# Performance work log

Measured on AMD Instinct MI355X. Metric: run time of the kernel, lower is better.

The kernel has to match this reference:

```python
import jax, jax.numpy as jnp
import numpy as np

D_MODEL = 512
N_HEADS = 8
HEAD_DIM = D_MODEL // N_HEADS
KV_RANK = 128
B, T = 8, 4096


def _rope(x):
    # x: (B, H, T, D); non-interleaved half rotation as in the source
    d = x.shape[-1]
    half = d // 2
    freq = 1.0 / (10000.0 ** (jnp.arange(half, dtype=jnp.float32) / half))
    t = jnp.arange(x.shape[2], dtype=jnp.float32)
    freqs = jnp.einsum('i,j->ij', t, freq)          # (T, half)
    cos_f = jnp.cos(freqs)[None, None, :, :]
    sin_f = jnp.sin(freqs)[None, None, :, :]
    x1, x2 = jnp.split(x, 2, axis=-1)
    return jnp.concatenate([x1 * cos_f - x2 * sin_f, x1 * sin_f + x2 * cos_f], axis=-1)


def setup_inputs() -> dict:
    key = jax.random.key(0)
    ks = jax.random.split(key, 9)
    s = lambda fan_in: 1.0 / np.sqrt(fan_in)
    return {
        'x':  jax.random.normal(ks[0], (B, T, D_MODEL), dtype=jnp.float32),
        'Wq': jax.random.normal(ks[1], (D_MODEL, D_MODEL), dtype=jnp.float32) * s(D_MODEL),
        'bq': jnp.zeros((D_MODEL,), dtype=jnp.float32),
        'Wd': jax.random.normal(ks[2], (D_MODEL, KV_RANK), dtype=jnp.float32) * s(D_MODEL),
        'bd': jnp.zeros((KV_RANK,), dtype=jnp.float32),
        'Wu': jax.random.normal(ks[3], (KV_RANK, D_MODEL * 2), dtype=jnp.float32) * s(KV_RANK),
        'bu': jnp.zeros((D_MODEL * 2,), dtype=jnp.float32),
        'Wo': jax.random.normal(ks[4], (D_MODEL, D_MODEL), dtype=jnp.float32) * s(D_MODEL),
        'bo': jnp.zeros((D_MODEL,), dtype=jnp.float32),
    }


def reference(x, Wq, bq, Wd, bd, Wu, bu, Wo, bo):
    b, t, _ = x.shape
    q = (x @ Wq + bq).reshape(b, t, N_HEADS, HEAD_DIM).transpose(0, 2, 1, 3)   # (B,H,T,D)
    kv = ((x @ Wd + bd) @ Wu + bu).reshape(b, t, N_HEADS, 2 * HEAD_DIM)
    k, v = jnp.split(kv, 2, axis=-1)
    k = k.transpose(0, 2, 1, 3)                                                # (B,H,T,D)
    v = v.transpose(0, 2, 1, 3)
    q = jax.nn.elu(_rope(q)) + 1.0
    k = jax.nn.elu(_rope(k)) + 1.0
    context = jnp.einsum('bhtd,bhte->bhde', k, v)      # (B,H,D,D)
    out = jnp.einsum('bhtd,bhde->bhte', q, context)    # (B,H,T,D)
    k_sum = k.sum(axis=2)                              # (B,H,D)
    z = 1.0 / (jnp.einsum('bhtd,bhd->bht', q, k_sum) + 1e-6)
    out = out * z[..., None]
    out = out.transpose(0, 2, 1, 3).reshape(b, t, D_MODEL)
    return out @ Wo + bo
```

## Files before the change

kernel.cpp:

```cpp
#include <hip/hip_runtime.h>
#include <math.h>

#define T_SEQ 4096
#define BATCH 8
#define DM    512
#define NH    8
#define HD    64
#define RANK  128
#define NCHUNK 8
#define MTOT  (BATCH * T_SEQ)
#define BK 64

typedef unsigned int u32;
typedef unsigned short u16;
using bf16x8  = __attribute__((ext_vector_type(8))) __bf16;
using floatx4 = __attribute__((ext_vector_type(4))) float;

__device__ __forceinline__ u16 f2bf(float f) {
  u32 u = __float_as_uint(f);
  u32 r = (u + 0x7FFFu + ((u >> 16) & 1u)) >> 16;
  return (u16)r;
}
__device__ __forceinline__ void hilo(float f, u16& h, u16& l) {
  h = f2bf(f);
  float hf = __uint_as_float(((u32)h) << 16);
  l = f2bf(f - hf);
}
__device__ __forceinline__ float elu1(float x) {
  return (x > 0.f) ? x + 1.f : expf(x);
}
__device__ __forceinline__ void async16(void* lds, const void* g) {
  __builtin_amdgcn_global_load_lds(
      (const __attribute__((address_space(1))) u32*)g,
      (__attribute__((address_space(3))) u32*)lds, 16, 0, 0);
}
__device__ __forceinline__ bf16x8 fragld(const u16* base, int row, int kk, int quad) {
  int ch = (kk * 4 + quad) ^ (row & 7);
  return *(const bf16x8*)((const char*)base + row * 128 + ch * 16);
}

__global__ void cs_kernel(float2* __restrict__ cs) {
  int i = blockIdx.x * 256 + threadIdx.x;
  if (i >= T_SEQ * 32) return;
  int t = i >> 5, d = i & 31;
  double freq = pow(10000.0, -(double)d / 32.0);
  double a = (double)t * freq;
  cs[i] = make_float2((float)cos(a), (float)sin(a));
}

__global__ __launch_bounds__(256) void pack_bf16(const float* __restrict__ x,
                                                 u16* __restrict__ y) {
  int i = blockIdx.x * 256 + threadIdx.x;
  const float4 v = ((const float4*)x)[i];
  ushort4 o;
  o.x = f2bf(v.x); o.y = f2bf(v.y); o.z = f2bf(v.z); o.w = f2bf(v.w);
  ((ushort4*)y)[i] = o;
}

__global__ __launch_bounds__(256) void transpose_cast(const float* __restrict__ W,
                                                      u16* __restrict__ WT,
                                                      int K, int N) {
  __shared__ float t[32][33];
  int kb = blockIdx.x * 32, nb = blockIdx.y * 32;
  int tx = threadIdx.x & 31, tg = threadIdx.x >> 5;
#pragma unroll
  for (int i = 0; i < 4; i++)
    t[tg * 4 + i][tx] = W[(size_t)(kb + tg * 4 + i) * N + nb + tx];
  __syncthreads();
#pragma unroll
  for (int i = 0; i < 4; i++)
    WT[(size_t)(nb + tg * 4 + i) * K + kb + tx] = f2bf(t[tx][tg * 4 + i]);
}

__global__ __launch_bounds__(256) void transpose_cast_hilo(
    const float* __restrict__ W, u16* __restrict__ WTh, u16* __restrict__ WTl,
    int K, int N) {
  __shared__ float t[32][33];
  int kb = blockIdx.x * 32, nb = blockIdx.y * 32;
  int tx = threadIdx.x & 31, tg = threadIdx.x >> 5;
#pragma unroll
  for (int i = 0; i < 4; i++)
    t[tg * 4 + i][tx] = W[(size_t)(kb + tg * 4 + i) * N + nb + tx];
  __syncthreads();
#pragma unroll
  for (int i = 0; i < 4; i++) {
    u16 h, l;
    hilo(t[tx][tg * 4 + i], h, l);
    WTh[(size_t)(nb + tg * 4 + i) * K + kb + tx] = h;
    WTl[(size_t)(nb + tg * 4 + i) * K + kb + tx] = l;
  }
}

template <bool BF16OUT>
__global__ __launch_bounds__(256) void gemm_bf16_bt(
    const u16* __restrict__ A, const u16* __restrict__ BT,
    const float* __restrict__ bias, void* __restrict__ Cv,
    int M, int N, int K) {
  __shared__ u16 As[128 * BK];
  __shared__ u16 Bs[128 * BK];
  const int tid = threadIdx.x;
  const int lane = tid & 63, w = tid >> 6;
  const int m0 = blockIdx.y * 128, n0 = blockIdx.x * 128;
  const int wm = (w & 1) * 64, wn = (w >> 1) * 64;
  const int srow = lane >> 3, schunk = lane & 7;
  const int lane15 = lane & 15, quad = lane >> 4;
  floatx4 acc[4][4] = {};
  for (int kt = 0; kt < K; kt += BK) {
    __syncthreads();
#pragma unroll
    for (int i = 0; i < 4; i++) {
      int R = (w * 4 + i) * 8 + srow;
      int cg = schunk ^ (R & 7);
      async16((char*)As + (w * 4 + i) * 1024,
              (const char*)A + ((size_t)(m0 + R) * K + kt) * 2 + cg * 16);
      async16((char*)Bs + (w * 4 + i) * 1024,
              (const char*)BT + ((size_t)(n0 + R) * K + kt) * 2 + cg * 16);
    }
    __syncthreads();
#pragma unroll
    for (int kk = 0; kk < 2; kk++) {
      bf16x8 af[4], bfr[4];
#pragma unroll
      for (int mi = 0; mi < 4; mi++) af[mi] = fragld(As, wm + mi * 16 + lane15, kk, quad);
#pragma unroll
      for (int ni = 0; ni < 4; ni++) bfr[ni] = fragld(Bs, wn + ni * 16 + lane15, kk, quad);
#pragma unroll
      for (int mi = 0; mi < 4; mi++)
#pragma unroll
        for (int ni = 0; ni < 4; ni++)
          acc[mi][ni] = __builtin_amdgcn_mfma_f32_16x16x32_bf16(
              af[mi], bfr[ni], acc[mi][ni], 0, 0, 0);
    }
  }
#pragma unroll
  for (int mi = 0; mi < 4; mi++) {
    int row = m0 + wm + mi * 16 + (quad << 2);
#pragma unroll
    for (int ni = 0; ni < 4; ni++) {
      int col = n0 + wn + ni * 16 + lane15;
      float bb = bias[col];
#pragma unroll
      for (int r = 0; r < 4; r++) {
        float v = acc[mi][ni][r] + bb;
        if (BF16OUT) ((u16*)Cv)[(size_t)(row + r) * N + col] = f2bf(v);
        else         ((float*)Cv)[(size_t)(row + r) * N + col] = v;
      }
    }
  }
}

__global__ __launch_bounds__(256) void gemm_wd_hilo(
    const u16* __restrict__ A, const u16* __restrict__ BT,
    const float* __restrict__ bias, u16* __restrict__ Ch, u16* __restrict__ Cl,
    int M, int N, int K) {
  __shared__ u16 As[128 * BK];
  __shared__ u16 Bs[128 * BK];
  const int tid = threadIdx.x;
  const int lane = tid & 63, w = tid >> 6;
  const int m0 = blockIdx.y * 128, n0 = blockIdx.x * 128;
  const int wm = (w & 1) * 64, wn = (w >> 1) * 64;
  const int srow = lane >> 3, schunk = lane & 7;
  const int lane15 = lane & 15, quad = lane >> 4;
  floatx4 acc[4][4] = {};
  for (int kt = 0; kt < K; kt += BK) {
    __syncthreads();
#pragma unroll
    for (int i = 0; i < 4; i++) {
      int R = (w * 4 + i) * 8 + srow;
      int cg = schunk ^ (R & 7);
      async16((char*)As + (w * 4 + i) * 1024,
              (const char*)A + ((size_t)(m0 + R) * K + kt) * 2 + cg * 16);
      async16((char*)Bs + (w * 4 + i) * 1024,
              (const char*)BT + ((size_t)(n0 + R) * K + kt) * 2 + cg * 16);
    }
    __syncthreads();
#pragma unroll
    for (int kk = 0; kk < 2; kk++) {
      bf16x8 af[4], bfr[4];
#pragma unroll
      for (int mi = 0; mi < 4; mi++) af[mi] = fragld(As, wm + mi * 16 + lane15, kk, quad);
#pragma unroll
      for (int ni = 0; ni < 4; ni++) bfr[ni] = fragld(Bs, wn + ni * 16 + lane15, kk, quad);
#pragma unroll
      for (int mi = 0; mi < 4; mi++)
#pragma unroll
        for (int ni = 0; ni < 4; ni++)
          acc[mi][ni] = __builtin_amdgcn_mfma_f32_16x16x32_bf16(
              af[mi], bfr[ni], acc[mi][ni], 0, 0, 0);
    }
  }
#pragma unroll
  for (int mi = 0; mi < 4; mi++) {
    int row = m0 + wm + mi * 16 + (quad << 2);
#pragma unroll
    for (int ni = 0; ni < 4; ni++) {
      int col = n0 + wn + ni * 16 + lane15;
      float bb = bias[col];
#pragma unroll
      for (int r = 0; r < 4; r++) {
        float v = acc[mi][ni][r] + bb;
        u16 hh, ll;
        hilo(v, hh, ll);
        size_t idx = (size_t)(row + r) * N + col;
        Ch[idx] = hh;
        Cl[idx] = ll;
      }
    }
  }
}

__global__ __launch_bounds__(256) void ctx_fused(
    const u16* __restrict__ Chi, const u16* __restrict__ Clo,
    const u16* __restrict__ Wuh, const u16* __restrict__ Wul,
    const float* __restrict__ bu, const float2* __restrict__ cs,
    float* __restrict__ ctxp, float* __restrict__ ksump) {
  __shared__ __align__(16) u16 uni[16384];
  __shared__ __align__(16) u16 Bh[128 * 64], Bl[128 * 64];
  __shared__ float bus[128];
  __shared__ float ksl[256];
  const int tid = threadIdx.x;
  const int lane = tid & 63, w = tid >> 6;
  const int lane15 = lane & 15, quad = lane >> 4;
  const int chunk = blockIdx.x, bh = blockIdx.y;
  const int b = bh >> 3, h = bh & 7;
  u16* Ah = uni;
  u16* Al = uni + 4096;
  u16* Kh = uni;
  u16* Kl = uni + 4096;
  u16* Vh = uni + 8192;
  u16* Vl = uni + 12288;
  if (tid < 128) bus[tid] = bu[h * RANK + tid];
  floatx4 acc2[4] = {};
  float ksacc[4] = {0.f, 0.f, 0.f, 0.f};
  for (int tile = 0; tile < 8; tile++) {
    const int t0 = chunk * 512 + tile * 64;
    floatx4 acc[8] = {};
#pragma unroll
    for (int rp = 0; rp < 2; rp++) {
      __syncthreads();
#pragma unroll
      for (int i = 0; i < 2; i++) {
        int R = (w * 2 + i) * 8 + (lane >> 3);
        int cg = (lane & 7) ^ (R & 7);
        size_t aoff = ((size_t)(b * T_SEQ + t0 + R) * RANK + rp * 64) * 2 + cg * 16;
        async16((char*)Ah + (w * 2 + i) * 1024, (const char*)Chi + aoff);
        async16((char*)Al + (w * 2 + i) * 1024, (const char*)Clo + aoff);
      }
#pragma unroll
      for (int i = 0; i < 4; i++) {
        int R = (w * 4 + i) * 8 + (lane >> 3);
        int cg = (lane & 7) ^ (R & 7);
        size_t boff = ((size_t)(h * 128 + R) * RANK + rp * 64) * 2 + cg * 16;
        async16((char*)Bh + (w * 4 + i) * 1024, (const char*)Wuh + boff);
        async16((char*)Bl + (w * 4 + i) * 1024, (const char*)Wul + boff);
      }
      __syncthreads();
#pragma unroll
      for (int kk = 0; kk < 2; kk++) {
        bf16x8 ah  = fragld(Ah, w * 16 + lane15, kk, quad);
        bf16x8 al8 = fragld(Al, w * 16 + lane15, kk, quad);
#pragma unroll
        for (int ni = 0; ni < 8; ni++) {
          bf16x8 bh8 = fragld(Bh, ni * 16 + lane15, kk, quad);
          bf16x8 bl8 = fragld(Bl, ni * 16 + lane15, kk, quad);
          acc[ni] = __builtin_amdgcn_mfma_f32_16x16x32_bf16(ah,  bh8, acc[ni], 0, 0, 0);
          acc[ni] = __builtin_amdgcn_mfma_f32_16x16x32_bf16(ah,  bl8, acc[ni], 0, 0, 0);
          acc[ni] = __builtin_amdgcn_mfma_f32_16x16x32_bf16(al8, bh8, acc[ni], 0, 0, 0);
          acc[ni] = __builtin_amdgcn_mfma_f32_16x16x32_bf16(al8, bl8, acc[ni], 0, 0, 0);
        }
      }
    }
    __syncthreads();
    {
      const int tloc = w * 16 + (quad << 2);
      const int tg = t0 + tloc;
      const int chq = w * 2 + (quad >> 1);
      const int half8 = (quad & 1) * 8;
#pragma unroll
      for (int ni = 0; ni < 2; ni++) {
        int d = ni * 16 + lane15;
        float b1 = bus[d], b2 = bus[d + 32];
        ushort4 khl, kll, khh, klh;
        float s0 = 0.f, s1 = 0.f;
#pragma unroll
        for (int r = 0; r < 4; r++) {
          float2 sc = cs[(size_t)(tg + r) * 32 + d];
          float x1 = acc[ni][r] + b1;
          float x2 = acc[ni + 2][r] + b2;
          float k1 = elu1(x1 * sc.x - x2 * sc.y);
          float k2 = elu1(x1 * sc.y + x2 * sc.x);
          s0 += k1; s1 += k2;
          u16 hh, ll;
          hilo(k1, hh, ll); ((u16*)&khl)[r] = hh; ((u16*)&kll)[r] = ll;
          hilo(k2, hh, ll); ((u16*)&khh)[r] = hh; ((u16*)&klh)[r] = ll;
        }
        ksacc[ni] += s0; ksacc[ni + 2] += s1;
        int offd = d * 128 + ((chq ^ (d & 7)) << 4) + half8;
        *(ushort4*)((char*)Kh + offd)              = khl;
        *(ushort4*)((char*)Kl + offd)              = kll;
        *(ushort4*)((char*)Kh + offd + 32 * 128)   = khh;
        *(ushort4*)((char*)Kl + offd + 32 * 128)   = klh;
      }
#pragma unroll
      for (int ni = 4; ni < 8; ni++) {
        int e = (ni - 4) * 16 + lane15;
        float be = bus[64 + e];
        ushort4 vh4, vl4;
#pragma unroll
        for (int r = 0; r < 4; r++) {
          u16 hh, ll;
          hilo(acc[ni][r] + be, hh, ll);
          ((u16*)&vh4)[r] = hh; ((u16*)&vl4)[r] = ll;
        }
        int off = e * 128 + ((chq ^ (e & 7)) << 4) + half8;
        *(ushort4*)((char*)Vh + off) = vh4;
        *(ushort4*)((char*)Vl + off) = vl4;
      }
    }
    __syncthreads();
#pragma unroll
    for (int kk = 0; kk < 2; kk++) {
      bf16x8 kh8 = fragld(Kh, w * 16 + lane15, kk, quad);
      bf16x8 kl8 = fragld(Kl, w * 16 + lane15, kk, quad);
#pragma unroll
      for (int ni = 0; ni < 4; ni++) {
        bf16x8 vh8 = fragld(Vh, ni * 16 + lane15, kk, quad);
        bf16x8 vl8 = fragld(Vl, ni * 16 + lane15, kk, quad);
        acc2[ni] = __builtin_amdgcn_mfma_f32_16x16x32_bf16(kh8, vh8, acc2[ni], 0, 0, 0);
        acc2[ni] = __builtin_amdgcn_mfma_f32_16x16x32_bf16(kh8, vl8, acc2[ni], 0, 0, 0);
        acc2[ni] = __builtin_amdgcn_mfma_f32_16x16x32_bf16(kl8, vh8, acc2[ni], 0, 0, 0);
        acc2[ni] = __builtin_amdgcn_mfma_f32_16x16x32_bf16(kl8, vl8, acc2[ni], 0, 0, 0);
      }
    }
  }
  const size_t obase = ((size_t)bh * NCHUNK + chunk) * 4096;
#pragma unroll
  for (int ni = 0; ni < 4; ni++)
#pragma unroll
    for (int r = 0; r < 4; r++)
      ctxp[obase + (size_t)(w * 16 + (quad << 2) + r) * 64 + ni * 16 + lane15] = acc2[ni][r];
  for (int g = 0; g < 4; g++) {
    __syncthreads();
    ksl[tid] = ksacc[g];
    __syncthreads();
    if (tid < 16) {
      float s = 0.f;
#pragma unroll
      for (int j = 0; j < 16; j++) s += ksl[(j >> 2) * 64 + (j & 3) * 16 + tid];
      ksump[(bh * NCHUNK + chunk) * 64 + g * 16 + tid] = s;
    }
  }
}

__global__ __launch_bounds__(256) void reduce_kernel(
    const float* __restrict__ ctxp, const float* __restrict__ ksump,
    float* __restrict__ ctx, float* __restrict__ ksum) {
  int bh = blockIdx.x, tid = threadIdx.x;
  for (int i = tid; i < 4096; i += 256) {
    float s = 0.f;
    for (int c = 0; c < NCHUNK; c++) s += ctxp[(size_t)(bh * NCHUNK + c) * 4096 + i];
    ctx[(size_t)bh * 4096 + i] = s;
  }
  if (tid < 64) {
    float s = 0.f;
    for (int c = 0; c < NCHUNK; c++) s += ksump[(bh * NCHUNK + c) * 64 + tid];
    ksum[bh * 64 + tid] = s;
  }
}

__global__ __launch_bounds__(256) void out_kernel(
    const float* __restrict__ Q, const float* __restrict__ ctx,
    const float* __restrict__ ksum, const float2* __restrict__ cs,
    u16* __restrict__ attn) {
  __shared__ __align__(16) float Qs[128 * 68];
  __shared__ __align__(16) float Cts[64 * 68];
  __shared__ float ks[64];
  __shared__ float zs[128];
  const int tid = threadIdx.x;
  const int tt0 = blockIdx.x * 128;
  const int bh = blockIdx.y;
  const int b = bh >> 3, h = bh & 7;
  for (int i = tid; i < 4096; i += 256)
    Cts[(i >> 6) * 68 + (i & 63)] = ctx[(size_t)bh * 4096 + i];
  if (tid < 64) ks[tid] = ksum[bh * 64 + tid];
  for (int i = tid; i < 8192; i += 256) {
    int t = i >> 6, d = i & 63;
    Qs[t * 68 + d] = Q[(size_t)(b * T_SEQ + tt0 + t) * DM + h * HD + d];
  }
  __syncthreads();
  for (int i = tid; i < 128 * 32; i += 256) {
    int t = i >> 5, d = i & 31;
    float x1 = Qs[t * 68 + d], x2 = Qs[t * 68 + d + 32];
    float2 sc = cs[(size_t)(tt0 + t) * 32 + d];
    float r1 = x1 * sc.x - x2 * sc.y;
    float r2 = x1 * sc.y + x2 * sc.x;
    Qs[t * 68 + d]      = (r1 > 0.f) ? r1 + 1.f : expf(r1);
    Qs[t * 68 + d + 32] = (r2 > 0.f) ? r2 + 1.f : expf(r2);
  }
  __syncthreads();
  if (tid < 128) {
    float z = 0.f;
#pragma unroll 8
    for (int d = 0; d < 64; d++) z += Qs[tid * 68 + d] * ks[d];
    zs[tid] = 1.f / (z + 1e-6f);
  }
  __syncthreads();
  const int tx = tid & 15, ty = tid >> 4;
  float acc[8][4] = {};
  for (int d = 0; d < 64; d++) {
    const float4 c4 = *(const float4*)&Cts[d * 68 + tx * 4];
#pragma unroll
    for (int i = 0; i < 8; i++) {
      float q = Qs[(ty * 8 + i) * 68 + d];
      acc[i][0] += q * c4.x; acc[i][1] += q * c4.y;
      acc[i][2] += q * c4.z; acc[i][3] += q * c4.w;
    }
  }
#pragma unroll
  for (int i = 0; i < 8; i++) {
    int t = ty * 8 + i;
    float zz = zs[t];
    ushort4 o;
    o.x = f2bf(acc[i][0] * zz); o.y = f2bf(acc[i][1] * zz);
    o.z = f2bf(acc[i][2] * zz); o.w = f2bf(acc[i][3] * zz);
    *(ushort4*)&attn[(size_t)(b * T_SEQ + tt0 + t) * DM + h * HD + tx * 4] = o;
  }
}

extern "C" void kernel_launch(void* const* d_in, const int* in_sizes, int n_in,
                              void* d_out, int out_size, void* d_ws, size_t ws_size,
                              hipStream_t stream) {
  const float* x  = (const float*)d_in[0];
  const float* Wq = (const float*)d_in[1];
  const float* bq = (const float*)d_in[2];
  const float* Wd = (const float*)d_in[3];
  const float* bd = (const float*)d_in[4];
  const float* Wu = (const float*)d_in[5];
  const float* bu = (const float*)d_in[6];
  const float* Wo = (const float*)d_in[7];
  const float* bo = (const float*)d_in[8];
  float* out = (float*)d_out;

  float* ws = (float*)d_ws;
  size_t o_cs   = 0;
  size_t o_Q    = o_cs + (size_t)T_SEQ * 32 * 2;
  size_t o_Chi  = o_Q + (size_t)MTOT * DM;
  size_t o_Clo  = o_Chi + (size_t)MTOT * RANK / 2;
  size_t o_ctxp = o_Clo + (size_t)MTOT * RANK / 2;
  size_t o_ksp  = o_ctxp + (size_t)64 * NCHUNK * 4096;
  size_t o_ctx  = o_ksp + (size_t)64 * NCHUNK * 64;
  size_t o_ks   = o_ctx + (size_t)64 * 4096;
  size_t o_xbf  = o_ks + 64 * 64;
  size_t o_wqT  = o_xbf + (size_t)MTOT * DM / 2;
  size_t o_wdT  = o_wqT + (size_t)DM * DM / 2;
  size_t o_woT  = o_wdT + (size_t)DM * RANK / 2;
  size_t o_wuTh = o_woT + (size_t)DM * DM / 2;
  size_t o_wuTl = o_wuTh + (size_t)(2 * DM) * RANK / 2;
  size_t total  = o_wuTl + (size_t)(2 * DM) * RANK / 2;
  if (ws_size < total * sizeof(float)) return;

  float2* cs  = (float2*)(ws + o_cs);
  float* Qb   = ws + o_Q;
  u16* Chi    = (u16*)(ws + o_Chi);
  u16* Clo    = (u16*)(ws + o_Clo);
  float* ctxp = ws + o_ctxp;
  float* ksp  = ws + o_ksp;
  float* ctxf = ws + o_ctx;
  float* ksf  = ws + o_ks;
  u16* x_bf   = (u16*)(ws + o_xbf);
  u16* attn_bf= x_bf;
  u16* WqT    = (u16*)(ws + o_wqT);
  u16* WdT    = (u16*)(ws + o_wdT);
  u16* WoT    = (u16*)(ws + o_woT);
  u16* WuTh   = (u16*)(ws + o_wuTh);
  u16* WuTl   = (u16*)(ws + o_wuTl);

  cs_kernel<<<(T_SEQ * 32 + 255) / 256, 256, 0, stream>>>(cs);
  pack_bf16<<<(MTOT * DM / 4) / 256, 256, 0, stream>>>(x, x_bf);
  transpose_cast<<<dim3(DM / 32, DM / 32), 256, 0, stream>>>(Wq, WqT, DM, DM);
  transpose_cast<<<dim3(DM / 32, RANK / 32), 256, 0, stream>>>(Wd, WdT, DM, RANK);
  transpose_cast<<<dim3(DM / 32, DM / 32), 256, 0, stream>>>(Wo, WoT, DM, DM);
  transpose_cast_hilo<<<dim3(RANK / 32, (2 * DM) / 32), 256, 0, stream>>>(
      Wu, WuTh, WuTl, RANK, 2 * DM);

  gemm_bf16_bt<false><<<dim3(DM / 128, MTOT / 128), 256, 0, stream>>>(
      x_bf, WqT, bq, Qb, MTOT, DM, DM);
  gemm_wd_hilo<<<dim3(RANK / 128, MTOT / 128), 256, 0, stream>>>(
      x_bf, WdT, bd, Chi, Clo, MTOT, RANK, DM);
  ctx_fused<<<dim3(NCHUNK, BATCH * NH), 256, 0, stream>>>(
      Chi, Clo, WuTh, WuTl, bu, cs, ctxp, ksp);
  reduce_kernel<<<BATCH * NH, 256, 0, stream>>>(ctxp, ksp, ctxf, ksf);
  out_kernel<<<dim3(T_SEQ / 128, BATCH * NH), 256, 0, stream>>>(Qb, ctxf, ksf, cs, attn_bf);
  gemm_bf16_bt<false><<<dim3(DM / 128, MTOT / 128), 256, 0, stream>>>(
      attn_bf, WoT, bo, out, MTOT, DM, DM);
}
```

Before: 323.5 us.

## Keep Wu fragments in registers and prefetch next A tile in ctx_fused

```diff
diff --git a/kernel.cpp b/kernel.cpp
--- a/kernel.cpp
+++ b/kernel.cpp
@@ -37,6 +37,10 @@
 __device__ __forceinline__ bf16x8 fragld(const u16* base, int row, int kk, int quad) {
   int ch = (kk * 4 + quad) ^ (row & 7);
   return *(const bf16x8*)((const char*)base + row * 128 + ch * 16);
+}
+__device__ __forceinline__ bf16x8 fragldA(const u16* base, int row, int gc) {
+  int ch = gc ^ (row & 7);
+  return *(const bf16x8*)((const char*)base + row * 256 + ch * 16);
 }
 
 __global__ void cs_kernel(float2* __restrict__ cs) {
@@ -209,13 +213,15 @@
   }
 }
 
-__global__ __launch_bounds__(256) void ctx_fused(
+__global__ __launch_bounds__(256, 2) void ctx_fused(
     const u16* __restrict__ Chi, const u16* __restrict__ Clo,
     const u16* __restrict__ Wuh, const u16* __restrict__ Wul,
     const float* __restrict__ bu, const float2* __restrict__ cs,
     float* __restrict__ ctxp, float* __restrict__ ksump) {
-  __shared__ __align__(16) u16 uni[16384];
-  __shared__ __align__(16) u16 Bh[128 * 64], Bl[128 * 64];
+  __shared__ __align__(16) u16 Ah_[64 * 128];
+  __shared__ __align__(16) u16 Al_[64 * 128];
+  __shared__ __align__(16) u16 Kh_[64 * 64], Kl_[64 * 64];
+  __shared__ __align__(16) u16 Vh_[64 * 64], Vl_[64 * 64];
   __shared__ float bus[128];
   __shared__ float ksl[256];
   const int tid = threadIdx.x;
@@ -223,70 +229,83 @@
   const int lane15 = lane & 15, quad = lane >> 4;
   const int chunk = blockIdx.x, bh = blockIdx.y;
   const int b = bh >> 3, h = bh & 7;
-  u16* Ah = uni;
-  u16* Al = uni + 4096;
-  u16* Kh = uni;
-  u16* Kl = uni + 4096;
-  u16* Vh = uni + 8192;
-  u16* Vl = uni + 12288;
   if (tid < 128) bus[tid] = bu[h * RANK + tid];
+
+  bf16x8 wuh[2][2][2], wul[2][2][2];
+  {
+    const int cb = (w >> 1) * 4 + (w & 1);
+#pragma unroll
+    for (int rp = 0; rp < 2; rp++)
+#pragma unroll
+      for (int kk = 0; kk < 2; kk++)
+#pragma unroll
+        for (int ct = 0; ct < 2; ct++) {
+          size_t off = (size_t)(h * 128 + (cb + ct * 2) * 16 + lane15) * RANK
+                       + rp * 64 + kk * 32 + quad * 8;
+          wuh[rp][kk][ct] = *(const bf16x8*)(Wuh + off);
+          wul[rp][kk][ct] = *(const bf16x8*)(Wul + off);
+        }
+  }
+
+  const int t00 = chunk * 512;
+  auto stageA = [&](int t0) {
+#pragma unroll
+    for (int i = 0; i < 4; i++) {
+      int R = i * 16 + w * 4 + (lane >> 4);
+      int cg = (lane & 15) ^ (R & 7);
+      size_t aoff = ((size_t)(b * T_SEQ + t0 + R) * RANK + cg * 8) * 2;
+      async16((char*)Ah_ + (i * 16 + w * 4) * 256, (const char*)Chi + aoff);
+      async16((char*)Al_ + (i * 16 + w * 4) * 256, (const char*)Clo + aoff);
+    }
+  };
+
   floatx4 acc2[4] = {};
-  float ksacc[4] = {0.f, 0.f, 0.f, 0.f};
+  float ks0 = 0.f, ks1 = 0.f;
+  stageA(t00);
   for (int tile = 0; tile < 8; tile++) {
-    const int t0 = chunk * 512 + tile * 64;
-    floatx4 acc[8] = {};
-#pragma unroll
-    for (int rp = 0; rp < 2; rp++) {
-      __syncthreads();
-#pragma unroll
-      for (int i = 0; i < 2; i++) {
-        int R = (w * 2 + i) * 8 + (lane >> 3);
-        int cg = (lane & 7) ^ (R & 7);
-        size_t aoff = ((size_t)(b * T_SEQ + t0 + R) * RANK + rp * 64) * 2 + cg * 16;
-        async16((char*)Ah + (w * 2 + i) * 1024, (const char*)Chi + aoff);
-        async16((char*)Al + (w * 2 + i) * 1024, (const char*)Clo + aoff);
+    const int t0 = t00 + tile * 64;
+    __syncthreads();
+    floatx4 acc[4][2] = {};
+#pragma unroll
+    for (int rp = 0; rp < 2; rp++)
+#pragma unroll
+      for (int kk = 0; kk < 2; kk++) {
+        const int gc = rp * 8 + kk * 4 + quad;
+        bf16x8 ah[4], al[4];
+#pragma unroll
+        for (int tt = 0; tt < 4; tt++) {
+          ah[tt] = fragldA(Ah_, tt * 16 + lane15, gc);
+          al[tt] = fragldA(Al_, tt * 16 + lane15, gc);
+        }
+#pragma unroll
+        for (int tt = 0; tt < 4; tt++)
+#pragma unroll
+          for (int ct = 0; ct < 2; ct++) {
+            acc[tt][ct] = __builtin_amdgcn_mfma_f32_16x16x32_bf16(
+                ah[tt], wuh[rp][kk][ct], acc[tt][ct], 0, 0, 0);
+            acc[tt][ct] = __builtin_amdgcn_mfma_f32_16x16x32_bf16(
+                ah[tt], wul[rp][kk][ct], acc[tt][ct], 0, 0, 0);
+            acc[tt][ct] = __builtin_amdgcn_mfma_f32_16x16x32_bf16(
+                al[tt], wuh[rp][kk][ct], acc[tt][ct], 0, 0, 0);
+            acc[tt][ct] = __builtin_amdgcn_mfma_f32_16x16x32_bf16(
+                al[tt], wul[rp][kk][ct], acc[tt][ct], 0, 0, 0);
+          }
       }
-#pragma unroll
-      for (int i = 0; i < 4; i++) {
-        int R = (w * 4 + i) * 8 + (lane >> 3);
-        int cg = (lane & 7) ^ (R & 7);
-        size_t boff = ((size_t)(h * 128 + R) * RANK + rp * 64) * 2 + cg * 16;
-        async16((char*)Bh + (w * 4 + i) * 1024, (const char*)Wuh + boff);
-        async16((char*)Bl + (w * 4 + i) * 1024, (const char*)Wul + boff);
-      }
-      __syncthreads();
-#pragma unroll
-      for (int kk = 0; kk < 2; kk++) {
-        bf16x8 ah  = fragld(Ah, w * 16 + lane15, kk, quad);
-        bf16x8 al8 = fragld(Al, w * 16 + lane15, kk, quad);
-#pragma unroll
-        for (int ni = 0; ni < 8; ni++) {
-          bf16x8 bh8 = fragld(Bh, ni * 16 + lane15, kk, quad);
-          bf16x8 bl8 = fragld(Bl, ni * 16 + lane15, kk, quad);
-          acc[ni] = __builtin_amdgcn_mfma_f32_16x16x32_bf16(ah,  bh8, acc[ni], 0, 0, 0);
-          acc[ni] = __builtin_amdgcn_mfma_f32_16x16x32_bf16(ah,  bl8, acc[ni], 0, 0, 0);
-          acc[ni] = __builtin_amdgcn_mfma_f32_16x16x32_bf16(al8, bh8, acc[ni], 0, 0, 0);
-          acc[ni] = __builtin_amdgcn_mfma_f32_16x16x32_bf16(al8, bl8, acc[ni], 0, 0, 0);
-        }
-      }
-    }
-    __syncthreads();
-    {
-      const int tloc = w * 16 + (quad << 2);
-      const int tg = t0 + tloc;
-      const int chq = w * 2 + (quad >> 1);
-      const int half8 = (quad & 1) * 8;
-#pragma unroll
-      for (int ni = 0; ni < 2; ni++) {
-        int d = ni * 16 + lane15;
-        float b1 = bus[d], b2 = bus[d + 32];
+    __syncthreads();
+    if (tile < 7) stageA(t0 + 64);
+    if (w < 2) {
+      const int d = w * 16 + lane15;
+      const float b1 = bus[d], b2 = bus[d + 32];
+#pragma unroll
+      for (int tt = 0; tt < 4; tt++) {
+        const int tg = t0 + tt * 16 + (quad << 2);
         ushort4 khl, kll, khh, klh;
         float s0 = 0.f, s1 = 0.f;
 #pragma unroll
         for (int r = 0; r < 4; r++) {
           float2 sc = cs[(size_t)(tg + r) * 32 + d];
-          float x1 = acc[ni][r] + b1;
-          float x2 = acc[ni + 2][r] + b2;
+          float x1 = acc[tt][0][r] + b1;
+          float x2 = acc[tt][1][r] + b2;
           float k1 = elu1(x1 * sc.x - x2 * sc.y);
           float k2 = elu1(x1 * sc.y + x2 * sc.x);
           s0 += k1; s1 += k2;
@@ -294,38 +313,45 @@
           hilo(k1, hh, ll); ((u16*)&khl)[r] = hh; ((u16*)&kll)[r] = ll;
           hilo(k2, hh, ll); ((u16*)&khh)[r] = hh; ((u16*)&klh)[r] = ll;
         }
-        ksacc[ni] += s0; ksacc[ni + 2] += s1;
-        int offd = d * 128 + ((chq ^ (d & 7)) << 4) + half8;
-        *(ushort4*)((char*)Kh + offd)              = khl;
-        *(ushort4*)((char*)Kl + offd)              = kll;
-        *(ushort4*)((char*)Kh + offd + 32 * 128)   = khh;
-        *(ushort4*)((char*)Kl + offd + 32 * 128)   = klh;
+        ks0 += s0; ks1 += s1;
+        const int chq = tt * 2 + (quad >> 1);
+        const int off = d * 128 + (((chq ^ (d & 7)) << 4) | ((quad & 1) << 3));
+        *(ushort4*)((char*)Kh_ + off)            = khl;
+        *(ushort4*)((char*)Kl_ + off)            = kll;
+        *(ushort4*)((char*)Kh_ + off + 32 * 128) = khh;
+        *(ushort4*)((char*)Kl_ + off + 32 * 128) = klh;
       }
-#pragma unroll
-      for (int ni = 4; ni < 8; ni++) {
-        int e = (ni - 4) * 16 + lane15;
-        float be = bus[64 + e];
-        ushort4 vh4, vl4;
-#pragma unroll
-        for (int r = 0; r < 4; r++) {
-          u16 hh, ll;
-          hilo(acc[ni][r] + be, hh, ll);
-          ((u16*)&vh4)[r] = hh; ((u16*)&vl4)[r] = ll;
+    } else {
+      const int e = (w - 2) * 16 + lane15;
+#pragma unroll
+      for (int ct = 0; ct < 2; ct++) {
+        const float be = bus[64 + e + ct * 32];
+#pragma unroll
+        for (int tt = 0; tt < 4; tt++) {
+          ushort4 vh4, vl4;
+#pragma unroll
+          for (int r = 0; r < 4; r++) {
+            u16 hh, ll;
+            hilo(acc[tt][ct][r] + be, hh, ll);
+            ((u16*)&vh4)[r] = hh; ((u16*)&vl4)[r] = ll;
+          }
+          const int chq = tt * 2 + (quad >> 1);
+          const int off = (e + ct * 32) * 128 +
+                          (((chq ^ (e & 7)) << 4) | ((quad & 1) << 3));
+          *(ushort4*)((char*)Vh_ + off) = vh4;
+          *(ushort4*)((char*)Vl_ + off) = vl4;
         }
-        int off = e * 128 + ((chq ^ (e & 7)) << 4) + half8;
-        *(ushort4*)((char*)Vh + off) = vh4;
-        *(ushort4*)((char*)Vl + off) = vl4;
       }
     }
     __syncthreads();
 #pragma unroll
     for (int kk = 0; kk < 2; kk++) {
-      bf16x8 kh8 = fragld(Kh, w * 16 + lane15, kk, quad);
-      bf16x8 kl8 = fragld(Kl, w * 16 + lane15, kk, quad);
+      bf16x8 kh8 = fragld(Kh_, w * 16 + lane15, kk, quad);
+      bf16x8 kl8 = fragld(Kl_, w * 16 + lane15, kk, quad);
 #pragma unroll
       for (int ni = 0; ni < 4; ni++) {
-        bf16x8 vh8 = fragld(Vh, ni * 16 + lane15, kk, quad);
-        bf16x8 vl8 = fragld(Vl, ni * 16 + lane15, kk, quad);
+        bf16x8 vh8 = fragld(Vh_, ni * 16 + lane15, kk, quad);
+        bf16x8 vl8 = fragld(Vl_, ni * 16 + lane15, kk, quad);
         acc2[ni] = __builtin_amdgcn_mfma_f32_16x16x32_bf16(kh8, vh8, acc2[ni], 0, 0, 0);
         acc2[ni] = __builtin_amdgcn_mfma_f32_16x16x32_bf16(kh8, vl8, acc2[ni], 0, 0, 0);
         acc2[ni] = __builtin_amdgcn_mfma_f32_16x16x32_bf16(kl8, vh8, acc2[ni], 0, 0, 0);
@@ -339,16 +365,18 @@
 #pragma unroll
     for (int r = 0; r < 4; r++)
       ctxp[obase + (size_t)(w * 16 + (quad << 2) + r) * 64 + ni * 16 + lane15] = acc2[ni][r];
-  for (int g = 0; g < 4; g++) {
-    __syncthreads();
-    ksl[tid] = ksacc[g];
-    __syncthreads();
-    if (tid < 16) {
-      float s = 0.f;
-#pragma unroll
-      for (int j = 0; j < 16; j++) s += ksl[(j >> 2) * 64 + (j & 3) * 16 + tid];
-      ksump[(bh * NCHUNK + chunk) * 64 + g * 16 + tid] = s;
-    }
+  if (w < 2) {
+    ksl[w * 128 + lane]      = ks0;
+    ksl[w * 128 + 64 + lane] = ks1;
+  }
+  __syncthreads();
+  if (tid < 64) {
+    const int d = tid;
+    const int wk = (d >> 4) & 1, hi = d >> 5, l15 = d & 15;
+    float s = 0.f;
+#pragma unroll
+    for (int q = 0; q < 4; q++) s += ksl[wk * 128 + hi * 64 + q * 16 + l15];
+    ksump[(bh * NCHUNK + chunk) * 64 + d] = s;
   }
 }
 
```

Measured after the change: 332.8 us. 2.9% more time.
